# Kernel optimization log

Hardware: AMD Instinct MI355X
Metric: run time of the kernel (lower is better)

## Reference

```python
import jax, jax.numpy as jnp
import numpy as np

B, T, F = 32, 4096, 512
H = 512

def setup_inputs() -> dict:
    key = jax.random.key(0)
    k1, k2, k3, k4, k5 = jax.random.split(key, 5)
    enc = jax.random.normal(k1, (B, T, F), dtype=jnp.float32)
    dec = jax.random.normal(k2, (B, F), dtype=jnp.float32)
    # Dense kernels (no bias), scaled like Glorot-ish init
    W1 = jax.random.normal(k3, (F, H), dtype=jnp.float32) / np.sqrt(F)
    W2 = jax.random.normal(k4, (F, H), dtype=jnp.float32) / np.sqrt(F)
    V = jax.random.normal(k5, (H, 1), dtype=jnp.float32) / np.sqrt(H)
    return {"encoder_outputs": enc, "dec_output": dec, "W1": W1, "W2": W2, "V": V}

def reference(encoder_outputs, dec_output, W1, W2, V):
    # Bahdanau additive attention, fully vectorized over time_steps
    # (the original runs this step-by-step via K.rnn; state is unchanged,
    # so the computation is embarrassingly parallel over t).
    w1_e = jnp.einsum('btf,fh->bth', encoder_outputs, W1)   # [B,T,H]
    w2_d = jnp.einsum('bf,fh->bh', dec_output, W2)          # [B,H]
    scores = jnp.einsum('bth,h->bt', jnp.tanh(w1_e + w2_d[:, None, :]), V[:, 0])  # [B,T]
    return jax.nn.softmax(scores, axis=1)
```

## Files before the change

kernel.cpp:

```cpp
#include <hip/hip_runtime.h>
#include <hip/hip_bf16.h>

#define B_ 32
#define T_ 4096
#define F_ 512
#define H_ 512

typedef float floatx4 __attribute__((ext_vector_type(4)));
typedef short short8 __attribute__((ext_vector_type(8)));

__device__ __forceinline__ unsigned short f2bf16(float a) {
  unsigned ua = __float_as_uint(a);
  return (unsigned short)((ua + 0x7FFFu + ((ua >> 16) & 1u)) >> 16);
}

__device__ __forceinline__ float tanh_fast(float x) {
  float e = __expf(2.0f * x);
  return 1.0f - __fdividef(2.0f, e + 1.0f);
}

__device__ __forceinline__ short8 cvt8(float4 lo, float4 hi) {
  union { short8 s8; __hip_bfloat16 h[8]; } u;
  u.h[0] = __float2bfloat16(lo.x);
  u.h[1] = __float2bfloat16(lo.y);
  u.h[2] = __float2bfloat16(lo.z);
  u.h[3] = __float2bfloat16(lo.w);
  u.h[4] = __float2bfloat16(hi.x);
  u.h[5] = __float2bfloat16(hi.y);
  u.h[6] = __float2bfloat16(hi.z);
  u.h[7] = __float2bfloat16(hi.w);
  return u.s8;
}

__global__ __launch_bounds__(1024) void prep_all(const float* __restrict__ W1,
                                                 unsigned short* __restrict__ W1T,
                                                 const float* __restrict__ dec,
                                                 const float* __restrict__ W2,
                                                 float* __restrict__ w2d) {
  __shared__ float tile[32][33];
  if (blockIdx.x < 256) {
    const int tx = threadIdx.x & 31, ty = threadIdx.x >> 5;
    const int bx = blockIdx.x & 15, by = blockIdx.x >> 4;
    const int f = by * 32 + ty;
    const int h = bx * 32 + tx;
    tile[ty][tx] = W1[f * H_ + h];
    __syncthreads();
    const int ho = bx * 32 + ty;
    const int fo = by * 32 + tx;
    W1T[ho * F_ + fo] = f2bf16(tile[tx][ty]);
  } else {
    const int g = (blockIdx.x - 256) * 1024 + threadIdx.x;
    const int b = g >> 9;
    const int h = g & 511;
    float s0 = 0.f, s1 = 0.f, s2 = 0.f, s3 = 0.f;
    for (int f = 0; f < F_; f += 4) {
      s0 += dec[b * F_ + f + 0] * W2[(f + 0) * H_ + h];
      s1 += dec[b * F_ + f + 1] * W2[(f + 1) * H_ + h];
      s2 += dec[b * F_ + f + 2] * W2[(f + 2) * H_ + h];
      s3 += dec[b * F_ + f + 3] * W2[(f + 3) * H_ + h];
    }
    w2d[b * H_ + h] = (s0 + s1) + (s2 + s3);
  }
}

__global__ __launch_bounds__(256, 4) void fused_score(
    const float* __restrict__ enc, const unsigned short* __restrict__ W1T,
    const float* __restrict__ w2d, const float* __restrict__ V,
    float* __restrict__ scores) {
  __shared__ __align__(16) unsigned short As[2][128 * 40];
  __shared__ __align__(16) unsigned short Bs[2][128 * 32];

  const int tid = threadIdx.x;
  const int bid = blockIdx.x;
  const int xcd = bid & 7;
  const int ii = bid >> 3;
  const int n_blk = ii & 3;
  const int m_blk = xcd + ((ii >> 2) << 3);
  const int lane = tid & 63;
  const int wave = tid >> 6;
  const int wm = wave >> 1;
  const int wn = wave & 1;
  const int quad = lane >> 4;
  const int l16 = lane & 15;

  const int arow = tid >> 2;
  const int acol = (tid & 3) * 8;
  const float* aptr = enc + (size_t)(m_blk * 128 + arow) * F_ + acol;

  const int nb0 = wave * 32;
  const int bl_n = lane >> 2;
  const int bl_c = (lane & 3) ^ (bl_n & 3);
  const unsigned short* bsrc0 =
      W1T + (size_t)(n_blk * 128 + nb0 + bl_n) * F_ + bl_c * 8;
  const unsigned short* bsrc1 = bsrc0 + 16 * F_;

  floatx4 acc[4][4];
#pragma unroll
  for (int i = 0; i < 4; i++)
#pragma unroll
    for (int j = 0; j < 4; j++) acc[i][j] = (floatx4){0.f, 0.f, 0.f, 0.f};

  float4 a_pre[4];

#pragma unroll
  for (int rr = 0; rr < 2; ++rr) {
    a_pre[rr * 2 + 0] = *(const float4*)(aptr + rr * 64 * F_ + 0);
    a_pre[rr * 2 + 1] = *(const float4*)(aptr + rr * 64 * F_ + 4);
  }
#pragma unroll
  for (int rr = 0; rr < 2; ++rr) {
    short8 pk = cvt8(a_pre[rr * 2 + 0], a_pre[rr * 2 + 1]);
    *(short8*)&As[0][(arow + rr * 64) * 40 + acol] = pk;
  }
  {
    __builtin_amdgcn_global_load_lds(
        (const __attribute__((address_space(1))) void*)bsrc0,
        (__attribute__((address_space(3))) void*)&Bs[0][nb0 * 32], 16, 0, 0);
    __builtin_amdgcn_global_load_lds(
        (const __attribute__((address_space(1))) void*)bsrc1,
        (__attribute__((address_space(3))) void*)&Bs[0][(nb0 + 16) * 32], 16, 0, 0);
  }
  __syncthreads();

  for (int ks = 0; ks < 16; ++ks) {
    const int cur = ks & 1;
    const int nxt = cur ^ 1;

    if (ks < 15) {
      const int k1 = (ks + 1) * 32;
#pragma unroll
      for (int rr = 0; rr < 2; ++rr) {
        a_pre[rr * 2 + 0] = *(const float4*)(aptr + rr * 64 * F_ + k1);
        a_pre[rr * 2 + 1] = *(const float4*)(aptr + rr * 64 * F_ + k1 + 4);
      }
      __builtin_amdgcn_global_load_lds(
          (const __attribute__((address_space(1))) void*)(bsrc0 + k1),
          (__attribute__((address_space(3))) void*)&Bs[nxt][nb0 * 32], 16, 0, 0);
      __builtin_amdgcn_global_load_lds(
          (const __attribute__((address_space(1))) void*)(bsrc1 + k1),
          (__attribute__((address_space(3))) void*)&Bs[nxt][(nb0 + 16) * 32], 16, 0, 0);
    }

    short8 af[4], bfr[4];
#pragma unroll
    for (int i = 0; i < 4; i++)
      af[i] = *(const short8*)&As[cur][(wm * 64 + i * 16 + l16) * 40 + quad * 8];
#pragma unroll
    for (int j = 0; j < 4; j++)
      bfr[j] = *(const short8*)&Bs[cur][(wn * 64 + j * 16 + l16) * 32 +
                                        ((quad ^ (l16 & 3)) * 8)];
#pragma unroll
    for (int i = 0; i < 4; i++)
#pragma unroll
      for (int j = 0; j < 4; j++)
        acc[i][j] = __builtin_amdgcn_mfma_f32_16x16x32_bf16(af[i], bfr[j], acc[i][j], 0, 0, 0);

    if (ks < 15) {
#pragma unroll
      for (int rr = 0; rr < 2; ++rr) {
        short8 pk = cvt8(a_pre[rr * 2 + 0], a_pre[rr * 2 + 1]);
        *(short8*)&As[nxt][(arow + rr * 64) * 40 + acol] = pk;
      }
    }
    __syncthreads();
  }

  const int b = m_blk >> 5;
  float w2v[4], vv[4];
#pragma unroll
  for (int j = 0; j < 4; j++) {
    const int h = n_blk * 128 + wn * 64 + j * 16 + l16;
    w2v[j] = w2d[b * H_ + h];
    vv[j] = V[h];
  }
  float rs[4][4];
#pragma unroll
  for (int i = 0; i < 4; i++)
#pragma unroll
    for (int r = 0; r < 4; r++) {
      float s = 0.f;
#pragma unroll
      for (int j = 0; j < 4; j++) s += tanh_fast(acc[i][j][r] + w2v[j]) * vv[j];
      rs[i][r] = s;
    }
#pragma unroll
  for (int i = 0; i < 4; i++)
#pragma unroll
    for (int r = 0; r < 4; r++) {
      float s = rs[i][r];
      s += __shfl_xor(s, 1, 16);
      s += __shfl_xor(s, 2, 16);
      s += __shfl_xor(s, 4, 16);
      s += __shfl_xor(s, 8, 16);
      rs[i][r] = s;
    }
  if (l16 == 0) {
#pragma unroll
    for (int i = 0; i < 4; i++)
#pragma unroll
      for (int r = 0; r < 4; r++)
        atomicAdd(&scores[m_blk * 128 + wm * 64 + i * 16 + quad * 4 + r], rs[i][r]);
  }
}

__global__ __launch_bounds__(256) void softmax_rows(const float* __restrict__ scores,
                                                    float* __restrict__ out) {
  const int b = blockIdx.x;
  const int tid = threadIdx.x;
  const int wave = tid >> 6;
  __shared__ float red[4];
  float v[16];
  float mx = -1e30f;
#pragma unroll
  for (int i = 0; i < 16; i++) {
    v[i] = scores[b * T_ + i * 256 + tid];
    mx = fmaxf(mx, v[i]);
  }
#pragma unroll
  for (int o = 32; o > 0; o >>= 1) mx = fmaxf(mx, __shfl_xor(mx, o, 64));
  if ((tid & 63) == 0) red[wave] = mx;
  __syncthreads();
  mx = fmaxf(fmaxf(red[0], red[1]), fmaxf(red[2], red[3]));
  __syncthreads();
  float sum = 0.f;
#pragma unroll
  for (int i = 0; i < 16; i++) {
    v[i] = __expf(v[i] - mx);
    sum += v[i];
  }
#pragma unroll
  for (int o = 32; o > 0; o >>= 1) sum += __shfl_xor(sum, o, 64);
  if ((tid & 63) == 0) red[wave] = sum;
  __syncthreads();
  sum = (red[0] + red[1]) + (red[2] + red[3]);
  const float inv = 1.0f / sum;
#pragma unroll
  for (int i = 0; i < 16; i++) out[b * T_ + i * 256 + tid] = v[i] * inv;
}

extern "C" void kernel_launch(void* const* d_in, const int* in_sizes, int n_in,
                              void* d_out, int out_size, void* d_ws, size_t ws_size,
                              hipStream_t stream) {
  const float* enc = (const float*)d_in[0];
  const float* dec = (const float*)d_in[1];
  const float* W1 = (const float*)d_in[2];
  const float* W2 = (const float*)d_in[3];
  const float* V = (const float*)d_in[4];
  float* out = (float*)d_out;

  char* ws = (char*)d_ws;
  float* scores = (float*)ws;
  unsigned short* W1T = (unsigned short*)(ws + 524288);
  float* w2d = (float*)(ws + 1048576);

  (void)in_sizes; (void)n_in; (void)out_size; (void)ws_size;

  hipMemsetAsync(scores, 0, B_ * T_ * sizeof(float), stream);
  prep_all<<<dim3(272), dim3(1024), 0, stream>>>(W1, W1T, dec, W2, w2d);
  fused_score<<<dim3(4096), dim3(256), 0, stream>>>(enc, W1T, w2d, V, scores);
  softmax_rows<<<dim3(32), dim3(256), 0, stream>>>(scores, out);
}
```

Before: 478.2 us.

## Triple-buffer W1 tiles with async LDS loads, fold memset into prep kernel

The B-operand (W1T) tiles now use three LDS buffers and are fetched two K-steps ahead via global_load_lds. The full __syncthreads is replaced by explicit partial vmcnt waits plus s_barrier, so in-flight loads can overlap the MFMA work. The LDS swizzle for B changes, the K loop is fully unrolled, and launch bounds drop to 3 blocks per CU to fit the extra LDS. The scores memset moves into extra blocks of prep_all, removing one launch, at the cost of lower occupancy and a vmcnt-based correctness dependency.

```diff
diff --git a/kernel.cpp b/kernel.cpp
--- a/kernel.cpp
+++ b/kernel.cpp
@@ -36,7 +36,8 @@
                                                  unsigned short* __restrict__ W1T,
                                                  const float* __restrict__ dec,
                                                  const float* __restrict__ W2,
-                                                 float* __restrict__ w2d) {
+                                                 float* __restrict__ w2d,
+                                                 float* __restrict__ scores) {
   __shared__ float tile[32][33];
   if (blockIdx.x < 256) {
     const int tx = threadIdx.x & 31, ty = threadIdx.x >> 5;
@@ -48,7 +49,7 @@
     const int ho = bx * 32 + ty;
     const int fo = by * 32 + tx;
     W1T[ho * F_ + fo] = f2bf16(tile[tx][ty]);
-  } else {
+  } else if (blockIdx.x < 272) {
     const int g = (blockIdx.x - 256) * 1024 + threadIdx.x;
     const int b = g >> 9;
     const int h = g & 511;
@@ -60,15 +61,20 @@
       s3 += dec[b * F_ + f + 3] * W2[(f + 3) * H_ + h];
     }
     w2d[b * H_ + h] = (s0 + s1) + (s2 + s3);
-  }
-}
-
-__global__ __launch_bounds__(256, 4) void fused_score(
+  } else {
+    const int g = (blockIdx.x - 272) * 1024 + threadIdx.x;
+    const float4 z = {0.f, 0.f, 0.f, 0.f};
+    ((float4*)scores)[g * 2 + 0] = z;
+    ((float4*)scores)[g * 2 + 1] = z;
+  }
+}
+
+__global__ __launch_bounds__(256, 3) void fused_score(
     const float* __restrict__ enc, const unsigned short* __restrict__ W1T,
     const float* __restrict__ w2d, const float* __restrict__ V,
     float* __restrict__ scores) {
   __shared__ __align__(16) unsigned short As[2][128 * 40];
-  __shared__ __align__(16) unsigned short Bs[2][128 * 32];
+  __shared__ __align__(16) unsigned short Bs[3][128 * 32];
 
   const int tid = threadIdx.x;
   const int bid = blockIdx.x;
@@ -89,7 +95,7 @@
 
   const int nb0 = wave * 32;
   const int bl_n = lane >> 2;
-  const int bl_c = (lane & 3) ^ (bl_n & 3);
+  const int bl_c = (lane & 3) ^ ((lane >> 3) & 3);
   const unsigned short* bsrc0 =
       W1T + (size_t)(n_blk * 128 + nb0 + bl_n) * F_ + bl_c * 8;
   const unsigned short* bsrc1 = bsrc0 + 16 * F_;
@@ -102,29 +108,32 @@
 
   float4 a_pre[4];
 
+#define GLDS(SRC, DST)                                                       \
+  __builtin_amdgcn_global_load_lds(                                          \
+      (const __attribute__((address_space(1))) void*)(SRC),                  \
+      (__attribute__((address_space(3))) void*)(DST), 16, 0, 0)
+
 #pragma unroll
   for (int rr = 0; rr < 2; ++rr) {
     a_pre[rr * 2 + 0] = *(const float4*)(aptr + rr * 64 * F_ + 0);
     a_pre[rr * 2 + 1] = *(const float4*)(aptr + rr * 64 * F_ + 4);
   }
+  GLDS(bsrc0, &Bs[0][nb0 * 32]);
+  GLDS(bsrc1, &Bs[0][(nb0 + 16) * 32]);
+  GLDS(bsrc0 + 32, &Bs[1][nb0 * 32]);
+  GLDS(bsrc1 + 32, &Bs[1][(nb0 + 16) * 32]);
 #pragma unroll
   for (int rr = 0; rr < 2; ++rr) {
     short8 pk = cvt8(a_pre[rr * 2 + 0], a_pre[rr * 2 + 1]);
     *(short8*)&As[0][(arow + rr * 64) * 40 + acol] = pk;
   }
-  {
-    __builtin_amdgcn_global_load_lds(
-        (const __attribute__((address_space(1))) void*)bsrc0,
-        (__attribute__((address_space(3))) void*)&Bs[0][nb0 * 32], 16, 0, 0);
-    __builtin_amdgcn_global_load_lds(
-        (const __attribute__((address_space(1))) void*)bsrc1,
-        (__attribute__((address_space(3))) void*)&Bs[0][(nb0 + 16) * 32], 16, 0, 0);
-  }
-  __syncthreads();
-
+  asm volatile("s_waitcnt vmcnt(2) lgkmcnt(0)" ::: "memory");
+  __builtin_amdgcn_s_barrier();
+
+#pragma unroll
   for (int ks = 0; ks < 16; ++ks) {
-    const int cur = ks & 1;
-    const int nxt = cur ^ 1;
+    const int cur3 = ks % 3;
+    const int cur2 = ks & 1;
 
     if (ks < 15) {
       const int k1 = (ks + 1) * 32;
@@ -133,22 +142,22 @@
         a_pre[rr * 2 + 0] = *(const float4*)(aptr + rr * 64 * F_ + k1);
         a_pre[rr * 2 + 1] = *(const float4*)(aptr + rr * 64 * F_ + k1 + 4);
       }
-      __builtin_amdgcn_global_load_lds(
-          (const __attribute__((address_space(1))) void*)(bsrc0 + k1),
-          (__attribute__((address_space(3))) void*)&Bs[nxt][nb0 * 32], 16, 0, 0);
-      __builtin_amdgcn_global_load_lds(
-          (const __attribute__((address_space(1))) void*)(bsrc1 + k1),
-          (__attribute__((address_space(3))) void*)&Bs[nxt][(nb0 + 16) * 32], 16, 0, 0);
+    }
+    if (ks < 14) {
+      const int nb3 = (ks + 2) % 3;
+      const int k2 = (ks + 2) * 32;
+      GLDS(bsrc0 + k2, &Bs[nb3][nb0 * 32]);
+      GLDS(bsrc1 + k2, &Bs[nb3][(nb0 + 16) * 32]);
     }
 
     short8 af[4], bfr[4];
 #pragma unroll
     for (int i = 0; i < 4; i++)
-      af[i] = *(const short8*)&As[cur][(wm * 64 + i * 16 + l16) * 40 + quad * 8];
+      af[i] = *(const short8*)&As[cur2][(wm * 64 + i * 16 + l16) * 40 + quad * 8];
 #pragma unroll
     for (int j = 0; j < 4; j++)
-      bfr[j] = *(const short8*)&Bs[cur][(wn * 64 + j * 16 + l16) * 32 +
-                                        ((quad ^ (l16 & 3)) * 8)];
+      bfr[j] = *(const short8*)&Bs[cur3][(wn * 64 + j * 16 + l16) * 32 +
+                                         ((quad ^ ((l16 >> 1) & 3)) * 8)];
 #pragma unroll
     for (int i = 0; i < 4; i++)
 #pragma unroll
@@ -159,11 +168,19 @@
 #pragma unroll
       for (int rr = 0; rr < 2; ++rr) {
         short8 pk = cvt8(a_pre[rr * 2 + 0], a_pre[rr * 2 + 1]);
-        *(short8*)&As[nxt][(arow + rr * 64) * 40 + acol] = pk;
+        *(short8*)&As[cur2 ^ 1][(arow + rr * 64) * 40 + acol] = pk;
       }
     }
-    __syncthreads();
-  }
+
+    if (ks < 14) {
+      asm volatile("s_waitcnt vmcnt(2) lgkmcnt(0)" ::: "memory");
+      __builtin_amdgcn_s_barrier();
+    } else if (ks == 14) {
+      asm volatile("s_waitcnt vmcnt(0) lgkmcnt(0)" ::: "memory");
+      __builtin_amdgcn_s_barrier();
+    }
+  }
+#undef GLDS
 
   const int b = m_blk >> 5;
   float w2v[4], vv[4];
@@ -255,8 +272,7 @@
 
   (void)in_sizes; (void)n_in; (void)out_size; (void)ws_size;
 
-  hipMemsetAsync(scores, 0, B_ * T_ * sizeof(float), stream);
-  prep_all<<<dim3(272), dim3(1024), 0, stream>>>(W1, W1T, dec, W2, w2d);
+  prep_all<<<dim3(288), dim3(1024), 0, stream>>>(W1, W1T, dec, W2, w2d, scores);
   fused_score<<<dim3(4096), dim3(256), 0, stream>>>(enc, W1T, w2d, V, scores);
   softmax_rows<<<dim3(32), dim3(256), 0, stream>>>(scores, out);
 }
```

New measurement: 513.3 us. 1.07x slower.
